# Kernel tuning notes

Hardware: AMD Instinct MI355X
Metric: run time of the kernel (lower is better)

Reference implementation:

```python
import jax, jax.numpy as jnp
import numpy as np

B, L, F, H, U = 512, 64, 2048, 512, 512


def setup_inputs() -> dict:
    key = jax.random.key(0)
    ks = jax.random.split(key, 10)
    s = 0.05
    return {
        'features': jax.random.normal(ks[0], (B, L, F), jnp.float32),
        'hidden': jax.random.normal(ks[1], (B, H), jnp.float32),
        'W1': jax.random.normal(ks[2], (F, U), jnp.float32) * s,
        'b1': jnp.zeros((U,), jnp.float32),
        'W2': jax.random.normal(ks[3], (H, U), jnp.float32) * s,
        'b2': jnp.zeros((U,), jnp.float32),
        'V': jax.random.normal(ks[4], (U, 1), jnp.float32) * s,
        'bV': jnp.zeros((1,), jnp.float32),
        'W3': jax.random.normal(ks[5], (F + H, U), jnp.float32) * s,
        'b3': jnp.zeros((U,), jnp.float32),
        'ka1': jax.random.normal(ks[6], (H, L), jnp.float32) * s,
        'kb1': jax.random.normal(ks[7], (L, L), jnp.float32) * s,
        'ka2': jax.random.normal(ks[8], (H, L), jnp.float32) * s,
        'kb2': jax.random.normal(ks[9], (L, L), jnp.float32) * s,
    }


def reference(features, hidden, W1, b1, W2, b2, V, bV, W3, b3, ka1, kb1, ka2, kb2):
    # features: [B, L, F], hidden: [B, H]
    Lp = features.shape[1]
    h = hidden[:, None, :]  # [B, 1, H] = hidden_with_time_axis

    # score_model == 'default'
    score = jnp.tanh(features @ W1 + b1 + (h @ W2 + b2))  # [B, L, U]
    logits = score @ V + bV  # [B, L, 1]
    attention_weights = jax.nn.softmax(logits, axis=1)  # [B, L, 1]

    # local_att == 'True': Gaussian window re-weighting (vectorized version of
    # the original nested Python loops over (batch, position)).
    def local_p(ka, kb):
        t = jnp.tanh(h @ ka) @ kb  # [B, 1, L]
        t = jax.nn.sigmoid(t) * jnp.sqrt(jnp.float32(Lp))
        return jnp.transpose(t, (0, 2, 1))  # [B, L, 1]

    p1 = local_p(ka1, kb1)  # predicted row center, [B, L, 1]
    p2 = local_p(ka2, kb2)  # predicted col center, [B, L, 1]

    i = jnp.arange(Lp, dtype=jnp.float32)
    g = jnp.sqrt(jnp.float32(Lp))
    rows = jnp.floor((i + 1.0) / g)                 # s_t[..., 0]
    cols = jnp.floor(jnp.mod(i + 1.0, g)) - 1.0     # s_t[..., 1]
    d2 = (rows[None, :, None] - p1) ** 2 + (cols[None, :, None] - p2) ** 2  # [B, L, 1]

    D = 1.0
    attention_weights = attention_weights * jnp.exp(-d2 / (0.5 * D * D))

    context_vector = jnp.sum(attention_weights * features, axis=1)  # [B, F]

    # context_vector_concat == 'True'
    out = jnp.tanh(jnp.concatenate([context_vector, hidden], axis=-1)) @ W3 + b3  # [B, U]
    return out, attention_weights
```

## Files before the change

### kernel.cpp

```cpp
#include <hip/hip_runtime.h>

typedef __bf16 bf16x8 __attribute__((ext_vector_type(8)));
typedef float f32x4 __attribute__((ext_vector_type(4)));

#define FAST_BARRIER()                                        \
  do {                                                        \
    asm volatile("s_waitcnt lgkmcnt(0)" ::: "memory");        \
    __builtin_amdgcn_s_barrier();                             \
    asm volatile("" ::: "memory");                            \
  } while (0)

static __device__ __forceinline__ unsigned short f2bf(float f) {
  union { float fv; unsigned u; } v; v.fv = f;
  unsigned u = v.u;
  u += 0x7fffu + ((u >> 16) & 1u);
  return (unsigned short)(u >> 16);
}

static __device__ __forceinline__ float fast_tanh(float x) {
  x = fminf(fmaxf(x, -15.f), 15.f);
  float ex = __expf(2.f * x);
  return (ex - 1.f) / (ex + 1.f);
}

__global__ __launch_bounds__(256) void pack_all(
    const float* __restrict__ W1, const float* __restrict__ W2,
    const float* __restrict__ W3,
    unsigned short* __restrict__ W1p, unsigned short* __restrict__ W2p,
    unsigned short* __restrict__ W3p) {
  __shared__ float tile[32][65];
  const int N = 512;
  const float* W; unsigned short* P; int nk;
  if (blockIdx.z == 0)      { W = W1; P = W1p; nk = 64; }
  else if (blockIdx.z == 1) { W = W2; P = W2p; nk = 16; }
  else                      { W = W3; P = W3p; nk = 80; }
  if ((int)blockIdx.x >= nk) return;
  int k0 = blockIdx.x * 32, n0 = blockIdx.y * 64;
  int t = threadIdx.x;
  int nn = t & 63, kkb = t >> 6;
#pragma unroll
  for (int i = 0; i < 8; ++i) {
    int kk = kkb + i * 4;
    tile[kk][nn] = W[(size_t)(k0 + kk) * N + n0 + nn];
  }
  __syncthreads();
#pragma unroll
  for (int i = 0; i < 8; ++i) {
    int e = t + i * 256;
    int k8 = e & 7, n = (e >> 3) & 63, c = e >> 9;
    size_t dst = (size_t)((k0 >> 3) + c) * 4096 + (size_t)(n0 + n) * 8 + k8;
    P[dst] = f2bf(tile[c * 8 + k8][n]);
  }
}

__global__ __launch_bounds__(128) void prep_batch(
    const float* __restrict__ hidden,
    const float* __restrict__ ka1, const float* __restrict__ kb1,
    const float* __restrict__ ka2, const float* __restrict__ kb2,
    float* __restrict__ gauss,
    unsigned short* __restrict__ hid_bf,
    unsigned short* __restrict__ A2) {
  int b = blockIdx.x, t = threadIdx.x;
  __shared__ float hl[512];
  __shared__ float tt[128];
  __shared__ float pp[128];
  for (int i = t; i < 512; i += 128) {
    float v = hidden[b * 512 + i];
    hl[i] = v;
    hid_bf[b * 512 + i] = f2bf(v);
    A2[(size_t)b * 2560 + 2048 + i] = f2bf(tanhf(v));
  }
  __syncthreads();
  {
    const float* ka = (t < 64) ? ka1 : ka2;
    int lp = t & 63;
    float s0 = 0.f, s1 = 0.f, s2 = 0.f, s3 = 0.f;
    for (int h = 0; h < 512; h += 4) {
      s0 += hl[h + 0] * ka[(h + 0) * 64 + lp];
      s1 += hl[h + 1] * ka[(h + 1) * 64 + lp];
      s2 += hl[h + 2] * ka[(h + 2) * 64 + lp];
      s3 += hl[h + 3] * ka[(h + 3) * 64 + lp];
    }
    tt[t] = tanhf((s0 + s1) + (s2 + s3));
  }
  __syncthreads();
  {
    const float* kb = (t < 64) ? kb1 : kb2;
    const float* ts = (t < 64) ? tt : tt + 64;
    int l = t & 63;
    float s = 0.f;
    for (int j = 0; j < 64; ++j) s += ts[j] * kb[j * 64 + l];
    pp[t] = 8.0f / (1.0f + expf(-s));
  }
  __syncthreads();
  if (t < 64) {
    float fi = (float)(t + 1);
    float r = floorf(fi * 0.125f);
    float c = floorf(fmodf(fi, 8.0f)) - 1.0f;
    float dr = r - pp[t], dc = c - pp[64 + t];
    gauss[b * 64 + t] = expf(-2.0f * (dr * dr + dc * dc));
  }
}

__global__ __launch_bounds__(256, 4) void gemm64d(
    const unsigned short* __restrict__ A, int lda, int k8_stride, int nsteps,
    const unsigned short* __restrict__ Wp,
    const float* __restrict__ bias,
    float* __restrict__ C) {
  __shared__ unsigned short lA[64 * 40];
  int m0 = blockIdx.x * 64, n0 = blockIdx.y * 64;
  int z = blockIdx.z;
  int k8 = z * k8_stride;
  int t = threadIdx.x;
  int w = t >> 6, lane = t & 63, q = lane >> 4, l15 = lane & 15;
  f32x4 acc[4] = {};
  int arow = t >> 2, achk = (t & 3) * 8;
  const unsigned short* pA = A + (size_t)(m0 + arow) * lda + (size_t)k8 * 8 + achk;
  const unsigned short* pB = Wp + ((size_t)(k8 + q) * 512 + n0 + w * 16 + l15) * 8;
  int4 av = *(const int4*)(pA);
  int4 bv = *(const int4*)(pB);
  for (int ks = 0; ks < nsteps; ++ks) {
    FAST_BARRIER();
    *(int4*)(lA + arow * 40 + achk) = av;
    FAST_BARRIER();
    int ksn = (ks + 1 < nsteps) ? ks + 1 : ks;
    av = *(const int4*)(pA + ksn * 32);
    int4 bn = *(const int4*)(pB + (size_t)ksn * 16384);
    bf16x8 bf = *(const bf16x8*)&bv;
#pragma unroll
    for (int mt = 0; mt < 4; ++mt) {
      bf16x8 af = *(const bf16x8*)(lA + (mt * 16 + l15) * 40 + q * 8);
      acc[mt] = __builtin_amdgcn_mfma_f32_16x16x32_bf16(af, bf, acc[mt], 0, 0, 0);
    }
    bv = bn;
  }
  int col = n0 + w * 16 + l15;
  if (bias) {
    float bsv = bias[col];
#pragma unroll
    for (int mt = 0; mt < 4; ++mt)
#pragma unroll
      for (int j = 0; j < 4; ++j)
        C[(size_t)(m0 + mt * 16 + q * 4 + j) * 512 + col] = acc[mt][j] + bsv;
  } else {
    float* Cp = C + (size_t)z * 262144;
#pragma unroll
    for (int mt = 0; mt < 4; ++mt)
#pragma unroll
      for (int j = 0; j < 4; ++j)
        Cp[(size_t)(m0 + mt * 16 + q * 4 + j) * 512 + col] = acc[mt][j];
  }
}

__global__ __launch_bounds__(256) void reduce4(const float* __restrict__ part,
                                               const float* __restrict__ b3,
                                               float* __restrict__ out) {
  int i = blockIdx.x * 256 + threadIdx.x;
  int base = i * 4;
  int n = base & 511;
  float4 p0 = *(const float4*)(part + base);
  float4 p1 = *(const float4*)(part + 262144 + base);
  float4 p2 = *(const float4*)(part + 524288 + base);
  float4 p3 = *(const float4*)(part + 786432 + base);
  float4 bv = *(const float4*)(b3 + n);
  float4 r;
  r.x = p0.x + p1.x + p2.x + p3.x + bv.x;
  r.y = p0.y + p1.y + p2.y + p3.y + bv.y;
  r.z = p0.z + p1.z + p2.z + p3.z + bv.z;
  r.w = p0.w + p1.w + p2.w + p3.w + bv.w;
  *(float4*)(out + base) = r;
}

__global__ __launch_bounds__(256, 2) void attn_main(
    const float* __restrict__ feat,
    const unsigned short* __restrict__ W1p,
    const float* __restrict__ b1,
    const float* __restrict__ hb,
    const float* __restrict__ V,
    const float* __restrict__ bVp,
    const float* __restrict__ gauss,
    float* __restrict__ aw_out,
    unsigned short* __restrict__ A2) {
  __shared__ unsigned short lA[2][64 * 40];
  __shared__ float red[64 * 4];
  __shared__ float awl[64];
  int b = blockIdx.x, t = threadIdx.x;
  int w = t >> 6, lane = t & 63, q = lane >> 4, l15 = lane & 15;
  f32x4 acc[4][8] = {};
  int row0 = t >> 3, ch0 = t & 7;
  const float* Ab = feat + (size_t)b * (64 * 2048);
  const float* pA0 = Ab + row0 * 2048 + ch0 * 4;
  const float* pA1 = pA0 + 32 * 2048;
  const unsigned short* pB = W1p + ((size_t)q * 512 + w * 128 + l15) * 8;
  int wA = row0 * 40 + ch0 * 4;

  auto mmaStep = [&](int buf, const int4* B) {
    __builtin_amdgcn_s_setprio(1);
#pragma unroll
    for (int mt = 0; mt < 4; ++mt) {
      bf16x8 af = *(const bf16x8*)(&lA[buf][(mt * 16 + l15) * 40 + q * 8]);
#pragma unroll
      for (int nt = 0; nt < 8; ++nt)
        acc[mt][nt] = __builtin_amdgcn_mfma_f32_16x16x32_bf16(
            af, *(const bf16x8*)&B[nt], acc[mt][nt], 0, 0, 0);
    }
    __builtin_amdgcn_s_setprio(0);
  };
  auto stage = [&](int buf, const float4& x0, const float4& x1) {
    ushort4 u0, u1;
    u0.x = f2bf(x0.x); u0.y = f2bf(x0.y); u0.z = f2bf(x0.z); u0.w = f2bf(x0.w);
    u1.x = f2bf(x1.x); u1.y = f2bf(x1.y); u1.z = f2bf(x1.z); u1.w = f2bf(x1.w);
    *(ushort4*)(&lA[buf][wA]) = u0;
    *(ushort4*)(&lA[buf][wA + 1280]) = u1;
  };

  int4 bc[8], bn[8];
  float4 a0, a1, na0, na1;
  a0 = *(const float4*)(pA0);
  a1 = *(const float4*)(pA1);
#pragma unroll
  for (int nt = 0; nt < 8; ++nt) bc[nt] = *(const int4*)(pB + nt * 128);
  stage(0, a0, a1);
  na0 = *(const float4*)(pA0 + 32);
  na1 = *(const float4*)(pA1 + 32);
#pragma unroll
  for (int nt = 0; nt < 8; ++nt) bn[nt] = *(const int4*)(pB + 16384 + nt * 128);
  FAST_BARRIER();

  for (int s2 = 0; s2 < 32; ++s2) {
    int s = 2 * s2;
    stage(1, na0, na1);
    {
      int kf = (s + 2 < 64) ? s + 2 : 63;
      a0 = *(const float4*)(pA0 + kf * 32);
      a1 = *(const float4*)(pA1 + kf * 32);
    }
    mmaStep(0, bc);
    {
      int kf = (s + 2 < 64) ? s + 2 : 63;
      const unsigned short* bp = pB + (size_t)kf * 16384;
#pragma unroll
      for (int nt = 0; nt < 8; ++nt) bc[nt] = *(const int4*)(bp + nt * 128);
    }
    FAST_BARRIER();
    stage(0, a0, a1);
    {
      int kf = (s + 3 < 64) ? s + 3 : 63;
      na0 = *(const float4*)(pA0 + kf * 32);
      na1 = *(const float4*)(pA1 + kf * 32);
    }
    mmaStep(1, bn);
    {
      int kf = (s + 3 < 64) ? s + 3 : 63;
      const unsigned short* bp = pB + (size_t)kf * 16384;
#pragma unroll
      for (int nt = 0; nt < 8; ++nt) bn[nt] = *(const int4*)(bp + nt * 128);
    }
    FAST_BARRIER();
  }

  float vv[8], bb[8];
#pragma unroll
  for (int nt = 0; nt < 8; ++nt) {
    int u = w * 128 + nt * 16 + l15;
    vv[nt] = V[u];
    bb[nt] = b1[u] + hb[b * 512 + u];
  }
  float gs = (t < 64) ? gauss[b * 64 + t] : 0.f;
  float bV0 = bVp[0];

#pragma unroll
  for (int mt = 0; mt < 4; ++mt) {
#pragma unroll
    for (int j = 0; j < 4; ++j) {
      float p = 0.f;
#pragma unroll
      for (int nt = 0; nt < 8; ++nt)
        p += fast_tanh(acc[mt][nt][j] + bb[nt]) * vv[nt];
      p += __shfl_xor(p, 1);
      p += __shfl_xor(p, 2);
      p += __shfl_xor(p, 4);
      p += __shfl_xor(p, 8);
      if (l15 == 0) red[(mt * 16 + q * 4 + j) * 4 + w] = p;
    }
  }
  __syncthreads();
  if (t < 64) {
    float s = bV0 + red[t * 4] + red[t * 4 + 1] + red[t * 4 + 2] + red[t * 4 + 3];
    float mx = s;
#pragma unroll
    for (int o = 1; o < 64; o <<= 1) mx = fmaxf(mx, __shfl_xor(mx, o));
    float e = __expf(s - mx);
    float sm = e;
#pragma unroll
    for (int o = 1; o < 64; o <<= 1) sm += __shfl_xor(sm, o);
    float a = (e / sm) * gs;
    awl[t] = a;
    aw_out[b * 64 + t] = a;
  }
  __syncthreads();
  float4 c0 = make_float4(0.f, 0.f, 0.f, 0.f);
  float4 c1 = make_float4(0.f, 0.f, 0.f, 0.f);
  const float* pF = Ab + t * 8;
  for (int l = 0; l < 64; ++l) {
    float a = awl[l];
    float4 f0 = *(const float4*)(pF + l * 2048);
    float4 f1 = *(const float4*)(pF + l * 2048 + 4);
    c0.x += a * f0.x; c0.y += a * f0.y; c0.z += a * f0.z; c0.w += a * f0.w;
    c1.x += a * f1.x; c1.y += a * f1.y; c1.z += a * f1.z; c1.w += a * f1.w;
  }
  ushort4 o0, o1;
  o0.x = f2bf(fast_tanh(c0.x)); o0.y = f2bf(fast_tanh(c0.y));
  o0.z = f2bf(fast_tanh(c0.z)); o0.w = f2bf(fast_tanh(c0.w));
  o1.x = f2bf(fast_tanh(c1.x)); o1.y = f2bf(fast_tanh(c1.y));
  o1.z = f2bf(fast_tanh(c1.z)); o1.w = f2bf(fast_tanh(c1.w));
  *(ushort4*)(A2 + (size_t)b * 2560 + t * 8) = o0;
  *(ushort4*)(A2 + (size_t)b * 2560 + t * 8 + 4) = o1;
}

extern "C" void kernel_launch(void* const* d_in, const int* in_sizes, int n_in,
                              void* d_out, int out_size, void* d_ws, size_t ws_size,
                              hipStream_t stream) {
  (void)in_sizes; (void)n_in; (void)out_size; (void)ws_size;
  const float* feat   = (const float*)d_in[0];
  const float* hidden = (const float*)d_in[1];
  const float* W1  = (const float*)d_in[2];
  const float* b1  = (const float*)d_in[3];
  const float* W2  = (const float*)d_in[4];
  const float* b2  = (const float*)d_in[5];
  const float* V   = (const float*)d_in[6];
  const float* bV  = (const float*)d_in[7];
  const float* W3  = (const float*)d_in[8];
  const float* b3  = (const float*)d_in[9];
  const float* ka1 = (const float*)d_in[10];
  const float* kb1 = (const float*)d_in[11];
  const float* ka2 = (const float*)d_in[12];
  const float* kb2 = (const float*)d_in[13];

  char* ws = (char*)d_ws;
  unsigned short* W3p   = (unsigned short*)(ws);
  unsigned short* A2    = (unsigned short*)(ws + 2621440);
  unsigned short* W1p   = (unsigned short*)(ws + 5242880);
  unsigned short* W2p   = (unsigned short*)(ws + 7340032);
  unsigned short* hidbf = (unsigned short*)(ws + 7864320);
  float*          hb    = (float*)(ws + 8388608);
  float*          gauss = (float*)(ws + 9437184);
  float*          part  = (float*)(ws + 5242880);

  float* out    = (float*)d_out;
  float* aw_out = out + 512 * 512;

  pack_all<<<dim3(80, 8, 3), 256, 0, stream>>>(W1, W2, W3, W1p, W2p, W3p);
  prep_batch<<<512, 128, 0, stream>>>(hidden, ka1, kb1, ka2, kb2, gauss, hidbf, A2);
  gemm64d<<<dim3(8, 8, 1), 256, 0, stream>>>(hidbf, 512, 0, 16, W2p, b2, hb);
  attn_main<<<512, 256, 0, stream>>>(feat, W1p, b1, hb, V, bV, gauss, aw_out, A2);
  gemm64d<<<dim3(8, 8, 4), 256, 0, stream>>>(A2, 2560, 80, 20, W3p, nullptr, part);
  reduce4<<<256, 256, 0, stream>>>(part, b3, out);
}
```

Measured before the change: 503.6 us.

## Fuse hidden@W2 into attention GEMM and load A fragments directly from global

Removes the separate hidden@W2 GEMM launch by appending 16 extra K-steps with hidden rows against packed W2 (contiguous after W1p) inside attn_main, broadcasting hidden to all rows. The A operand is now loaded straight from global into registers and converted to bf16 in registers, dropping the LDS staging buffer and the barriers. prep_batch is widened to 512 threads with a split-K reduction for the ka projections. The cost is more redundant global loads of features per wave and extra MFMA work for the hidden term.

```diff
diff --git a/kernel.cpp b/kernel.cpp
--- a/kernel.cpp
+++ b/kernel.cpp
@@ -21,6 +21,13 @@
   x = fminf(fmaxf(x, -15.f), 15.f);
   float ex = __expf(2.f * x);
   return (ex - 1.f) / (ex + 1.f);
+}
+
+static __device__ __forceinline__ bf16x8 cvt8(const float4& a, const float4& b) {
+  bf16x8 r;
+  r[0] = (__bf16)a.x; r[1] = (__bf16)a.y; r[2] = (__bf16)a.z; r[3] = (__bf16)a.w;
+  r[4] = (__bf16)b.x; r[5] = (__bf16)b.y; r[6] = (__bf16)b.z; r[7] = (__bf16)b.w;
+  return r;
 }
 
 __global__ __launch_bounds__(256) void pack_all(
@@ -53,38 +60,43 @@
   }
 }
 
-__global__ __launch_bounds__(128) void prep_batch(
+__global__ __launch_bounds__(512) void prep_batch(
     const float* __restrict__ hidden,
     const float* __restrict__ ka1, const float* __restrict__ kb1,
     const float* __restrict__ ka2, const float* __restrict__ kb2,
     float* __restrict__ gauss,
-    unsigned short* __restrict__ hid_bf,
     unsigned short* __restrict__ A2) {
   int b = blockIdx.x, t = threadIdx.x;
   __shared__ float hl[512];
+  __shared__ float part[512];
   __shared__ float tt[128];
   __shared__ float pp[128];
-  for (int i = t; i < 512; i += 128) {
-    float v = hidden[b * 512 + i];
-    hl[i] = v;
-    hid_bf[b * 512 + i] = f2bf(v);
-    A2[(size_t)b * 2560 + 2048 + i] = f2bf(tanhf(v));
-  }
-  __syncthreads();
   {
-    const float* ka = (t < 64) ? ka1 : ka2;
+    float v = hidden[b * 512 + t];
+    hl[t] = v;
+    A2[(size_t)b * 2560 + 2048 + t] = f2bf(tanhf(v));
+  }
+  __syncthreads();
+  {
+    const float* ka = (t < 256) ? ka1 : ka2;
     int lp = t & 63;
+    int h0 = ((t >> 6) & 3) * 128;
     float s0 = 0.f, s1 = 0.f, s2 = 0.f, s3 = 0.f;
-    for (int h = 0; h < 512; h += 4) {
+    for (int h = h0; h < h0 + 128; h += 4) {
       s0 += hl[h + 0] * ka[(h + 0) * 64 + lp];
       s1 += hl[h + 1] * ka[(h + 1) * 64 + lp];
       s2 += hl[h + 2] * ka[(h + 2) * 64 + lp];
       s3 += hl[h + 3] * ka[(h + 3) * 64 + lp];
     }
-    tt[t] = tanhf((s0 + s1) + (s2 + s3));
-  }
-  __syncthreads();
-  {
+    part[t] = (s0 + s1) + (s2 + s3);
+  }
+  __syncthreads();
+  if (t < 128) {
+    int base = ((t >= 64) ? 256 : 0) + (t & 63);
+    tt[t] = tanhf(part[base] + part[base + 64] + part[base + 128] + part[base + 192]);
+  }
+  __syncthreads();
+  if (t < 128) {
     const float* kb = (t < 64) ? kb1 : kb2;
     const float* ts = (t < 64) ? tt : tt + 64;
     int l = t & 63;
@@ -175,88 +187,70 @@
     const float* __restrict__ feat,
     const unsigned short* __restrict__ W1p,
     const float* __restrict__ b1,
-    const float* __restrict__ hb,
+    const float* __restrict__ b2,
+    const float* __restrict__ hidden,
     const float* __restrict__ V,
     const float* __restrict__ bVp,
     const float* __restrict__ gauss,
     float* __restrict__ aw_out,
     unsigned short* __restrict__ A2) {
-  __shared__ unsigned short lA[2][64 * 40];
   __shared__ float red[64 * 4];
   __shared__ float awl[64];
   int b = blockIdx.x, t = threadIdx.x;
   int w = t >> 6, lane = t & 63, q = lane >> 4, l15 = lane & 15;
   f32x4 acc[4][8] = {};
-  int row0 = t >> 3, ch0 = t & 7;
   const float* Ab = feat + (size_t)b * (64 * 2048);
-  const float* pA0 = Ab + row0 * 2048 + ch0 * 4;
-  const float* pA1 = pA0 + 32 * 2048;
+  const float* pAr = Ab + l15 * 2048 + q * 8;
+  const float* ph  = hidden + b * 512 + q * 8;
   const unsigned short* pB = W1p + ((size_t)q * 512 + w * 128 + l15) * 8;
-  int wA = row0 * 40 + ch0 * 4;
-
-  auto mmaStep = [&](int buf, const int4* B) {
-    __builtin_amdgcn_s_setprio(1);
+
+  float4 fc[8];
+#pragma unroll
+  for (int mt = 0; mt < 4; ++mt) {
+    fc[2 * mt]     = *(const float4*)(pAr + mt * 32768);
+    fc[2 * mt + 1] = *(const float4*)(pAr + mt * 32768 + 4);
+  }
+  bf16x8 af[4];
+#pragma unroll
+  for (int mt = 0; mt < 4; ++mt) af[mt] = cvt8(fc[2 * mt], fc[2 * mt + 1]);
+
+  for (int s = 0; s < 64; ++s) {
+    int kf = (s + 1 < 64) ? s + 1 : 63;
+    float4 fn[8];
+    const float* ap = pAr + kf * 32;
 #pragma unroll
     for (int mt = 0; mt < 4; ++mt) {
-      bf16x8 af = *(const bf16x8*)(&lA[buf][(mt * 16 + l15) * 40 + q * 8]);
+      fn[2 * mt]     = *(const float4*)(ap + mt * 32768);
+      fn[2 * mt + 1] = *(const float4*)(ap + mt * 32768 + 4);
+    }
+    const unsigned short* bp = pB + (size_t)s * 16384;
+    int4 bc[8];
+#pragma unroll
+    for (int nt = 0; nt < 8; ++nt) bc[nt] = *(const int4*)(bp + nt * 128);
+#pragma unroll
+    for (int mt = 0; mt < 4; ++mt)
 #pragma unroll
       for (int nt = 0; nt < 8; ++nt)
         acc[mt][nt] = __builtin_amdgcn_mfma_f32_16x16x32_bf16(
-            af, *(const bf16x8*)&B[nt], acc[mt][nt], 0, 0, 0);
-    }
-    __builtin_amdgcn_s_setprio(0);
-  };
-  auto stage = [&](int buf, const float4& x0, const float4& x1) {
-    ushort4 u0, u1;
-    u0.x = f2bf(x0.x); u0.y = f2bf(x0.y); u0.z = f2bf(x0.z); u0.w = f2bf(x0.w);
-    u1.x = f2bf(x1.x); u1.y = f2bf(x1.y); u1.z = f2bf(x1.z); u1.w = f2bf(x1.w);
-    *(ushort4*)(&lA[buf][wA]) = u0;
-    *(ushort4*)(&lA[buf][wA + 1280]) = u1;
-  };
-
-  int4 bc[8], bn[8];
-  float4 a0, a1, na0, na1;
-  a0 = *(const float4*)(pA0);
-  a1 = *(const float4*)(pA1);
-#pragma unroll
-  for (int nt = 0; nt < 8; ++nt) bc[nt] = *(const int4*)(pB + nt * 128);
-  stage(0, a0, a1);
-  na0 = *(const float4*)(pA0 + 32);
-  na1 = *(const float4*)(pA1 + 32);
-#pragma unroll
-  for (int nt = 0; nt < 8; ++nt) bn[nt] = *(const int4*)(pB + 16384 + nt * 128);
-  FAST_BARRIER();
-
-  for (int s2 = 0; s2 < 32; ++s2) {
-    int s = 2 * s2;
-    stage(1, na0, na1);
-    {
-      int kf = (s + 2 < 64) ? s + 2 : 63;
-      a0 = *(const float4*)(pA0 + kf * 32);
-      a1 = *(const float4*)(pA1 + kf * 32);
-    }
-    mmaStep(0, bc);
-    {
-      int kf = (s + 2 < 64) ? s + 2 : 63;
-      const unsigned short* bp = pB + (size_t)kf * 16384;
-#pragma unroll
-      for (int nt = 0; nt < 8; ++nt) bc[nt] = *(const int4*)(bp + nt * 128);
-    }
-    FAST_BARRIER();
-    stage(0, a0, a1);
-    {
-      int kf = (s + 3 < 64) ? s + 3 : 63;
-      na0 = *(const float4*)(pA0 + kf * 32);
-      na1 = *(const float4*)(pA1 + kf * 32);
-    }
-    mmaStep(1, bn);
-    {
-      int kf = (s + 3 < 64) ? s + 3 : 63;
-      const unsigned short* bp = pB + (size_t)kf * 16384;
-#pragma unroll
-      for (int nt = 0; nt < 8; ++nt) bn[nt] = *(const int4*)(bp + nt * 128);
-    }
-    FAST_BARRIER();
+            af[mt], *(const bf16x8*)&bc[nt], acc[mt][nt], 0, 0, 0);
+#pragma unroll
+    for (int mt = 0; mt < 4; ++mt) af[mt] = cvt8(fn[2 * mt], fn[2 * mt + 1]);
+  }
+
+  for (int s2 = 0; s2 < 16; ++s2) {
+    float4 ha  = *(const float4*)(ph + s2 * 32);
+    float4 hb4 = *(const float4*)(ph + s2 * 32 + 4);
+    const unsigned short* bp = pB + (size_t)(64 + s2) * 16384;
+    int4 bt[8];
+#pragma unroll
+    for (int nt = 0; nt < 8; ++nt) bt[nt] = *(const int4*)(bp + nt * 128);
+    bf16x8 ah = cvt8(ha, hb4);
+#pragma unroll
+    for (int mt = 0; mt < 4; ++mt)
+#pragma unroll
+      for (int nt = 0; nt < 8; ++nt)
+        acc[mt][nt] = __builtin_amdgcn_mfma_f32_16x16x32_bf16(
+            ah, *(const bf16x8*)&bt[nt], acc[mt][nt], 0, 0, 0);
   }
 
   float vv[8], bb[8];
@@ -264,7 +258,7 @@
   for (int nt = 0; nt < 8; ++nt) {
     int u = w * 128 + nt * 16 + l15;
     vv[nt] = V[u];
-    bb[nt] = b1[u] + hb[b * 512 + u];
+    bb[nt] = b1[u] + b2[u];
   }
   float gs = (t < 64) ? gauss[b * 64 + t] : 0.f;
   float bV0 = bVp[0];
@@ -304,10 +298,10 @@
   const float* pF = Ab + t * 8;
   for (int l = 0; l < 64; ++l) {
     float a = awl[l];
-    float4 f0 = *(const float4*)(pF + l * 2048);
-    float4 f1 = *(const float4*)(pF + l * 2048 + 4);
-    c0.x += a * f0.x; c0.y += a * f0.y; c0.z += a * f0.z; c0.w += a * f0.w;
-    c1.x += a * f1.x; c1.y += a * f1.y; c1.z += a * f1.z; c1.w += a * f1.w;
+    float4 g0 = *(const float4*)(pF + l * 2048);
+    float4 g1 = *(const float4*)(pF + l * 2048 + 4);
+    c0.x += a * g0.x; c0.y += a * g0.y; c0.z += a * g0.z; c0.w += a * g0.w;
+    c1.x += a * g1.x; c1.y += a * g1.y; c1.z += a * g1.z; c1.w += a * g1.w;
   }
   ushort4 o0, o1;
   o0.x = f2bf(fast_tanh(c0.x)); o0.y = f2bf(fast_tanh(c0.y));
@@ -342,8 +336,6 @@
   unsigned short* A2    = (unsigned short*)(ws + 2621440);
   unsigned short* W1p   = (unsigned short*)(ws + 5242880);
   unsigned short* W2p   = (unsigned short*)(ws + 7340032);
-  unsigned short* hidbf = (unsigned short*)(ws + 7864320);
-  float*          hb    = (float*)(ws + 8388608);
   float*          gauss = (float*)(ws + 9437184);
   float*          part  = (float*)(ws + 5242880);
 
@@ -351,9 +343,8 @@
   float* aw_out = out + 512 * 512;
 
   pack_all<<<dim3(80, 8, 3), 256, 0, stream>>>(W1, W2, W3, W1p, W2p, W3p);
-  prep_batch<<<512, 128, 0, stream>>>(hidden, ka1, kb1, ka2, kb2, gauss, hidbf, A2);
-  gemm64d<<<dim3(8, 8, 1), 256, 0, stream>>>(hidbf, 512, 0, 16, W2p, b2, hb);
-  attn_main<<<512, 256, 0, stream>>>(feat, W1p, b1, hb, V, bV, gauss, aw_out, A2);
+  prep_batch<<<512, 512, 0, stream>>>(hidden, ka1, kb1, ka2, kb2, gauss, A2);
+  attn_main<<<512, 256, 0, stream>>>(feat, W1p, b1, b2, hidden, V, bV, gauss, aw_out, A2);
   gemm64d<<<dim3(8, 8, 4), 256, 0, stream>>>(A2, 2560, 80, 20, W3p, nullptr, part);
   reduce4<<<256, 256, 0, stream>>>(part, b3, out);
 }
```

After: 558.5 us. 1.11x slower.
